# Kernel tuning notes

Hardware: AMD Instinct MI355X
Metric: run time of the kernel (lower is better)

## Reference

```python
import jax, jax.numpy as jnp
import numpy as np

# --- constants matching DILConfig ---
N_DIFF = 1000      # num_diffusion_steps
STEPS = 4          # inference_steps
S_MAX = 4          # max_scales
BUDGET = 0.2       # entropy_budget
G0 = 2.0           # guidance_strength
ENT_LO = 0.1       # stability_threshold_low
ENT_HI = 0.5       # stability_threshold_high
B, L, C, H = 16, 1024, 128, 512


def setup_inputs() -> dict:
    key = jax.random.key(0)
    ks = jax.random.split(key, 6)
    y_obs = jax.random.normal(ks[0], (B, L, C), dtype=jnp.float32)
    mask = (jax.random.uniform(ks[1], (B, L, C)) > 0.5).astype(jnp.float32)
    z_init = jax.random.normal(ks[2], (B, L, C), dtype=jnp.float32)
    W1 = jax.random.normal(ks[3], (C, H), dtype=jnp.float32) / np.sqrt(C)
    b1 = jnp.zeros((H,), dtype=jnp.float32)
    W2 = jax.random.normal(ks[4], (H, C), dtype=jnp.float32) / np.sqrt(H)
    b2 = jnp.zeros((C,), dtype=jnp.float32)
    tw = jax.random.normal(ks[5], (H,), dtype=jnp.float32)
    return {"y_obs": y_obs, "mask": mask, "z_init": z_init,
            "W1": W1, "b1": b1, "W2": W2, "b2": b2, "tw": tw}


def _dil_forward(y_obs, mask, z_init, W1, b1, W2, b2, tw):
    # diffusion schedule (linear betas)
    betas = jnp.linspace(1e-4, 0.02, N_DIFF, dtype=jnp.float32)
    ac = jnp.cumprod(1.0 - betas)
    alpha = jnp.sqrt(ac)                     # sqrt_alphas_cumprod
    sigma = jnp.sqrt(1.0 - ac)               # sqrt_one_minus_alphas_cumprod
    lam = jnp.log(alpha) - jnp.log(sigma)    # log-SNR/2

    step = N_DIFF // STEPS
    ks = [N_DIFF - 1 - i * step for i in range(STEPS)]

    def score(z, k):
        # epsilon predictor: channel MLP with scalar time feature
        t_feat = jnp.float32(k) / N_DIFF
        h = jax.nn.gelu(jnp.einsum('blc,ch->blh', z, W1) + b1 + t_feat * tw)
        return jnp.einsum('blh,hc->blc', h, W2) + b2

    z = z_init
    for k in ks:  # fixed small unrolled loop over inference steps
        kp = max(k - step, 0)
        eps = score(z, k)                                   # [B,L,C]
        h_lam = lam[kp] - lam[k]
        base_a = alpha[kp] / alpha[k]
        base_b = sigma[kp] * (jnp.exp(h_lam) - 1.0)

        # entropy map: batch-mean |eps| per pixel
        ent_pix = jnp.mean(jnp.abs(eps), axis=0)            # [L,C]

        # self-guidance on observed entries
        obs_err = (z - y_obs) * mask
        guidance = -obs_err / (jnp.var(obs_err) + 1e-8)     # [B,L,C]

        z_new = z
        # coarse -> fine so finer-scale selected nodes overwrite coarser ones
        for s in range(S_MAX - 1, -1, -1):
            w = 2 ** s
            pooled = ent_pix.reshape(L // w, w, C // w, w).mean(axis=(1, 3))
            Knodes = max(1, int(BUDGET * pooled.size))
            _, idx = jax.lax.top_k(pooled.ravel(), Knodes)
            selg = jnp.zeros((pooled.size,), jnp.float32).at[idx].set(1.0)
            selg = selg.reshape(pooled.shape)
            sel = jnp.repeat(jnp.repeat(selg, w, axis=0), w, axis=1)     # [L,C]
            ent_up = jnp.repeat(jnp.repeat(pooled, w, axis=0), w, axis=1)

            # adaptive solver order from entropy stability thresholds
            order = (1.0 + (ent_up > ENT_LO).astype(jnp.float32)
                         + (ent_up > ENT_HI).astype(jnp.float32))
            corr = (1.0 + (order - 1.0) * 0.5 * h_lam
                        + (order - 1.0) * (order - 2.0) / 6.0 * h_lam ** 2)
            gs = G0 * ent_up / (ent_up + 1.0)               # adaptive guidance

            cand = base_a * z - base_b * (corr * eps) + gs * guidance
            z_new = jnp.where(sel[None, :, :] > 0, cand, z_new)
        z = z_new
    return z


def reference(y_obs, mask, z_init, W1, b1, W2, b2, tw):
    return _dil_forward(y_obs, mask, z_init, W1, b1, W2, b2, tw)
```

## Files before the change

kernel.cpp:

```cpp
#include <hip/hip_runtime.h>
#include <math.h>
#include <stdint.h>

#define L_DIM 1024
#define C_DIM 128
#define H_DIM 512
#define B_DIM 16
#define LC (L_DIM * C_DIM)
#define BLC (B_DIM * LC)
#define M_DIM (B_DIM * L_DIM)

typedef __attribute__((ext_vector_type(8))) short short8;
typedef __attribute__((ext_vector_type(4))) float floatx4;

__device__ __forceinline__ unsigned ford(float x) {
    unsigned u = __float_as_uint(x);
    return (u & 0x80000000u) ? ~u : (u | 0x80000000u);
}

__device__ __forceinline__ void split3(float x, unsigned& uh, unsigned& um,
                                       unsigned& ul) {
    uh = __float_as_uint(x);
    const float r1 = x - __uint_as_float(uh & 0xffff0000u);
    um = __float_as_uint(r1);
    const float r2 = r1 - __uint_as_float(um & 0xffff0000u);
    ul = __float_as_uint(r2);
}

__device__ __forceinline__ float gelu_fast(float x) {
    const float g = 0.7978845608028654f * (x + 0.044715f * x * x * x);
    const float e = __expf(2.0f * g);
    const float t = 1.0f - 2.0f / (e + 1.0f);
    return 0.5f * x * (1.0f + t);
}

__global__ __launch_bounds__(256) void wsplit_kernel(
    const float* __restrict__ W1, const float* __restrict__ W2,
    unsigned short* __restrict__ W1h, unsigned short* __restrict__ W1m,
    unsigned short* __restrict__ W1l, unsigned short* __restrict__ W2h,
    unsigned short* __restrict__ W2m, unsigned short* __restrict__ W2l) {
    const int t = blockIdx.x * 256 + threadIdx.x;
    unsigned uh, um, ul;
    if (t < 65536) {
        const int j = t & 7, lane = (t >> 3) & 63, nt = (t >> 9) & 31,
                  kt = (t >> 14) & 3;
        const int k = kt * 32 + (lane >> 4) * 8 + j;
        const int n = nt * 16 + (lane & 15);
        split3(W1[k * 512 + n], uh, um, ul);
        W1h[t] = (unsigned short)(uh >> 16);
        W1m[t] = (unsigned short)(um >> 16);
        W1l[t] = (unsigned short)(ul >> 16);
    } else {
        const int t2 = t - 65536;
        const int j = t2 & 7, lane = (t2 >> 3) & 63, nt = (t2 >> 9) & 7,
                  kt = (t2 >> 12) & 15;
        const int k = kt * 32 + (lane >> 4) * 8 + j;
        const int n = nt * 16 + (lane & 15);
        split3(W2[k * 128 + n], uh, um, ul);
        W2h[t2] = (unsigned short)(uh >> 16);
        W2m[t2] = (unsigned short)(um >> 16);
        W2l[t2] = (unsigned short)(ul >> 16);
    }
}

#define MFMA6(AH, AM, AL, BH, BM, BL, ACC)                                    \
    ACC = __builtin_amdgcn_mfma_f32_16x16x32_bf16(AL, BH, ACC, 0, 0, 0);      \
    ACC = __builtin_amdgcn_mfma_f32_16x16x32_bf16(AM, BM, ACC, 0, 0, 0);      \
    ACC = __builtin_amdgcn_mfma_f32_16x16x32_bf16(AH, BL, ACC, 0, 0, 0);      \
    ACC = __builtin_amdgcn_mfma_f32_16x16x32_bf16(AM, BH, ACC, 0, 0, 0);      \
    ACC = __builtin_amdgcn_mfma_f32_16x16x32_bf16(AH, BM, ACC, 0, 0, 0);      \
    ACC = __builtin_amdgcn_mfma_f32_16x16x32_bf16(AH, BH, ACC, 0, 0, 0);

__device__ __forceinline__ void ldsA(const unsigned* hm,
                                     const unsigned short* lr, int row,
                                     int kbase, short8& Ah, short8& Am,
                                     short8& Al) {
    const unsigned* p = &hm[row * 132 + kbase];
    const uint4 a = *(const uint4*)p;
    const uint4 b = *(const uint4*)(p + 4);
    union { short8 v; unsigned u[4]; } ah, am;
    ah.u[0] = (a.x & 0xffffu) | (a.y << 16);
    ah.u[1] = (a.z & 0xffffu) | (a.w << 16);
    ah.u[2] = (b.x & 0xffffu) | (b.y << 16);
    ah.u[3] = (b.z & 0xffffu) | (b.w << 16);
    am.u[0] = (a.x >> 16) | (a.y & 0xffff0000u);
    am.u[1] = (a.z >> 16) | (a.w & 0xffff0000u);
    am.u[2] = (b.x >> 16) | (b.y & 0xffff0000u);
    am.u[3] = (b.z >> 16) | (b.w & 0xffff0000u);
    Ah = ah.v;
    Am = am.v;
    Al = *(const short8*)(&lr[row * 136 + kbase]);
}

__global__ __launch_bounds__(512, 2) void mlp_kernel(
    const float* __restrict__ z, const float* __restrict__ y,
    const float* __restrict__ mk,
    const unsigned short* __restrict__ W1h, const unsigned short* __restrict__ W1m,
    const unsigned short* __restrict__ W1l, const unsigned short* __restrict__ W2h,
    const unsigned short* __restrict__ W2m, const unsigned short* __restrict__ W2l,
    const float* __restrict__ b1, const float* __restrict__ tw,
    const float* __restrict__ b2, float t_feat,
    float* __restrict__ eps_out, float* __restrict__ ent,
    float* __restrict__ accum) {
    __shared__ unsigned z_hm[32 * 132];
    __shared__ unsigned short z_l[32 * 136];
    __shared__ unsigned h_hm[32 * 132];
    __shared__ unsigned short h_l[32 * 136];
    __shared__ float red1[8], red2[8];
    const int tid = threadIdx.x;
    const int w = tid >> 6, lane = tid & 63;
    const int quad = lane >> 4, m16 = lane & 15;
    const int l0 = blockIdx.x * 2;

#pragma unroll
    for (int e = 0; e < 2; ++e) {
        const int f = tid * 8 + e * 4;
        const int r = f >> 7, c = f & 127;
        const int b = r & 15, il = r >> 4;
        const float4 v = *(const float4*)(z + ((size_t)b * 1024 + l0 + il) * 128 + c);
        const float xs[4] = {v.x, v.y, v.z, v.w};
#pragma unroll
        for (int i = 0; i < 4; ++i) {
            unsigned uh, um, ul;
            split3(xs[i], uh, um, ul);
            z_hm[r * 132 + c + i] = (uh >> 16) | (um & 0xffff0000u);
            z_l[r * 136 + c + i] = (unsigned short)(ul >> 16);
        }
    }
    __syncthreads();

    floatx4 acc2[2];
    acc2[0] = (floatx4){0.f, 0.f, 0.f, 0.f};
    acc2[1] = (floatx4){0.f, 0.f, 0.f, 0.f};

    for (int hf = 0; hf < 2; ++hf) {
        floatx4 acc1[4];
#pragma unroll
        for (int i = 0; i < 4; ++i) acc1[i] = (floatx4){0.f, 0.f, 0.f, 0.f};

#pragma unroll
        for (int kt = 0; kt < 4; ++kt) {
            short8 Ah[2], Am[2], Al[2];
#pragma unroll
            for (int il = 0; il < 2; ++il)
                ldsA(z_hm, z_l, il * 16 + m16, kt * 32 + quad * 8,
                     Ah[il], Am[il], Al[il]);
#pragma unroll
            for (int s = 0; s < 2; ++s) {
                const int nt1 = (hf * 2 + s) * 8 + w;
                const size_t off = ((size_t)(kt * 32 + nt1) * 64 + lane) * 8;
                const short8 bh = *(const short8*)(W1h + off);
                const short8 bm = *(const short8*)(W1m + off);
                const short8 bl = *(const short8*)(W1l + off);
#pragma unroll
                for (int il = 0; il < 2; ++il) {
                    floatx4 a = acc1[s * 2 + il];
                    MFMA6(Ah[il], Am[il], Al[il], bh, bm, bl, a);
                    acc1[s * 2 + il] = a;
                }
            }
        }

#pragma unroll
        for (int s = 0; s < 2; ++s) {
            const int q = hf * 2 + s;
            __syncthreads();
            {
                const int coll = w * 16 + m16;
                const int colg = q * 128 + coll;
                const float bb = b1[colg] + t_feat * tw[colg];
#pragma unroll
                for (int il = 0; il < 2; ++il) {
#pragma unroll
                    for (int r = 0; r < 4; ++r) {
                        const float x = gelu_fast(acc1[s * 2 + il][r] + bb);
                        unsigned uh, um, ul;
                        split3(x, uh, um, ul);
                        const int row = il * 16 + quad * 4 + r;
                        h_hm[row * 132 + coll] = (uh >> 16) | (um & 0xffff0000u);
                        h_l[row * 136 + coll] = (unsigned short)(ul >> 16);
                    }
                }
            }
            __syncthreads();

#pragma unroll
            for (int ktl = 0; ktl < 4; ++ktl) {
                short8 Ah2[2], Am2[2], Al2[2];
#pragma unroll
                for (int il = 0; il < 2; ++il)
                    ldsA(h_hm, h_l, il * 16 + m16, ktl * 32 + quad * 8,
                         Ah2[il], Am2[il], Al2[il]);
                const int ktg = q * 4 + ktl;
                const size_t off = ((size_t)(ktg * 8 + w) * 64 + lane) * 8;
                const short8 bh = *(const short8*)(W2h + off);
                const short8 bm = *(const short8*)(W2m + off);
                const short8 bl = *(const short8*)(W2l + off);
#pragma unroll
                for (int il = 0; il < 2; ++il) {
                    floatx4 a = acc2[il];
                    MFMA6(Ah2[il], Am2[il], Al2[il], bh, bm, bl, a);
                    acc2[il] = a;
                }
            }
        }
    }

    {
        const int col = w * 16 + m16;
        const float bb2 = b2[col];
#pragma unroll
        for (int il = 0; il < 2; ++il) {
            float pa = 0.f;
#pragma unroll
            for (int r = 0; r < 4; ++r) {
                const float e = acc2[il][r] + bb2;
                const int b = quad * 4 + r;
                eps_out[((size_t)b * 1024 + l0 + il) * 128 + col] = e;
                pa += fabsf(e);
            }
            pa += __shfl_xor(pa, 16);
            pa += __shfl_xor(pa, 32);
            if (quad == 0) ent[(l0 + il) * 128 + col] = pa * (1.0f / 16.0f);
        }
    }

    float s1 = 0.f, s2 = 0.f;
#pragma unroll
    for (int e = 0; e < 2; ++e) {
        const int f = tid * 8 + e * 4;
        const int r = f >> 7, c = f & 127;
        const int b = r & 15, il = r >> 4;
        const size_t g = ((size_t)b * 1024 + l0 + il) * 128 + c;
        const float4 zv = *(const float4*)(z + g);
        const float4 yv = *(const float4*)(y + g);
        const float4 mv = *(const float4*)(mk + g);
        float oe;
        oe = (zv.x - yv.x) * mv.x; s1 += oe; s2 += oe * oe;
        oe = (zv.y - yv.y) * mv.y; s1 += oe; s2 += oe * oe;
        oe = (zv.z - yv.z) * mv.z; s1 += oe; s2 += oe * oe;
        oe = (zv.w - yv.w) * mv.w; s1 += oe; s2 += oe * oe;
    }
#pragma unroll
    for (int off = 32; off; off >>= 1) {
        s1 += __shfl_down(s1, off);
        s2 += __shfl_down(s2, off);
    }
    if (lane == 0) { red1[w] = s1; red2[w] = s2; }
    __syncthreads();
    if (tid == 0) {
        float a1 = 0.f, a2 = 0.f;
#pragma unroll
        for (int i = 0; i < 8; ++i) { a1 += red1[i]; a2 += red2[i]; }
        atomicAdd(&accum[0], a1);
        atomicAdd(&accum[1], a2);
    }
}

__global__ __launch_bounds__(256) void pool_kernel(
    const float* __restrict__ ent, float* __restrict__ p1,
    float* __restrict__ p2, float* __restrict__ p3) {
    const int idx = blockIdx.x * 256 + threadIdx.x;
    if (idx < 32768) {
        const int r = idx >> 6, c = idx & 63;
        float s = 0.f;
#pragma unroll
        for (int i = 0; i < 2; ++i)
#pragma unroll
            for (int j = 0; j < 2; ++j) s += ent[((r * 2 + i) << 7) + c * 2 + j];
        p1[idx] = s * 0.25f;
    } else if (idx < 40960) {
        const int t = idx - 32768;
        const int r = t >> 5, c = t & 31;
        float s = 0.f;
#pragma unroll
        for (int i = 0; i < 4; ++i)
#pragma unroll
            for (int j = 0; j < 4; ++j) s += ent[((r * 4 + i) << 7) + c * 4 + j];
        p2[t] = s * 0.0625f;
    } else {
        const int t = idx - 40960;
        const int r = t >> 4, c = t & 15;
        float s = 0.f;
#pragma unroll
        for (int i = 0; i < 8; ++i)
#pragma unroll
            for (int j = 0; j < 8; ++j) s += ent[((r * 8 + i) << 7) + c * 8 + j];
        p3[t] = s * (1.0f / 64.0f);
    }
}

__global__ __launch_bounds__(256) void hist_kernel(
    const float* __restrict__ e0, const float* __restrict__ e1,
    const float* __restrict__ e2, const float* __restrict__ e3,
    unsigned* __restrict__ ghist, unsigned* __restrict__ gprefix,
    unsigned* __restrict__ gkrem, unsigned* __restrict__ dctr, int shift) {
    const int bid = blockIdx.x;
    const float* data;
    int scale, base;
    if (bid < 64) { scale = 0; data = e0; base = bid * 2048; }
    else if (bid < 80) { scale = 1; data = e1; base = (bid - 64) * 2048; }
    else if (bid < 84) { scale = 2; data = e2; base = (bid - 80) * 2048; }
    else { scale = 3; data = e3; base = 0; }

    __shared__ unsigned hist[4][256];
    __shared__ unsigned sh[256];
    __shared__ bool sh_last;
    const int t = threadIdx.x;
    const int w = t >> 6;
#pragma unroll
    for (int i = t; i < 1024; i += 256) ((unsigned*)hist)[i] = 0u;
    __syncthreads();

    const unsigned prefix = gprefix[scale];
    const unsigned hmask = (shift == 24) ? 0u : (0xFFFFFFFFu << (shift + 8));

#pragma unroll
    for (int i = t; i < 2048; i += 256) {
        const unsigned u = ford(data[base + i]);
        if ((u & hmask) == (prefix & hmask))
            atomicAdd(&hist[w][(u >> shift) & 255u], 1u);
    }
    __syncthreads();
    const unsigned c = hist[0][t] + hist[1][t] + hist[2][t] + hist[3][t];
    if (c) atomicAdd(&ghist[scale * 256 + t], c);
    __syncthreads();

    if (t == 0) {
        __threadfence();
        sh_last = (atomicAdd(dctr, 1u) == 84u);
    }
    __syncthreads();
    if (!sh_last) return;

    __threadfence();
    const unsigned Kc[4] = {26214u, 6553u, 1638u, 409u};
#pragma unroll
    for (int s = 0; s < 4; ++s) {
        sh[t] = atomicAdd(&ghist[s * 256 + t], 0u);
        __syncthreads();
#pragma unroll
        for (int off = 1; off < 256; off <<= 1) {
            const unsigned v = (t + off < 256) ? sh[t + off] : 0u;
            __syncthreads();
            sh[t] += v;
            __syncthreads();
        }
        const unsigned suf = sh[t];
        const unsigned sufn = (t < 255) ? sh[t + 1] : 0u;
        const unsigned krem = (shift == 24) ? Kc[s] : gkrem[s];
        const unsigned pref = (shift == 24) ? 0u : gprefix[s];
        if (suf >= krem && sufn < krem) {
            gprefix[s] = pref | ((unsigned)t << shift);
            gkrem[s] = krem - sufn;
        }
        ghist[s * 256 + t] = 0u;
        __syncthreads();
    }
}

__global__ __launch_bounds__(256) void update_kernel(
    float* __restrict__ z, const float* __restrict__ y,
    const float* __restrict__ mk, const float* __restrict__ eps,
    const float* __restrict__ ent, const float* __restrict__ p1,
    const float* __restrict__ p2, const float* __restrict__ p3,
    const unsigned* __restrict__ thr, const float* __restrict__ accum,
    float base_a, float base_b, float h_lam) {
    const int idx = blockIdx.x * 256 + threadIdx.x;
    const int p = idx & (LC - 1);
    const int l = p >> 7;
    const int c = p & 127;

    const float mean = accum[0] * (1.0f / (float)BLC);
    const float var = accum[1] * (1.0f / (float)BLC) - mean * mean;

    const float zi = z[idx];
    const float oe = (zi - y[idx]) * mk[idx];
    const float guid = -oe / (var + 1e-8f);
    const float ei = eps[idx];

    float ent_v = 0.f;
    bool sel = false;
    {
        const float v0 = ent[p];
        if (ford(v0) >= thr[0]) { ent_v = v0; sel = true; }
        else {
            const float v1 = p1[((l >> 1) << 6) + (c >> 1)];
            if (ford(v1) >= thr[1]) { ent_v = v1; sel = true; }
            else {
                const float v2 = p2[((l >> 2) << 5) + (c >> 2)];
                if (ford(v2) >= thr[2]) { ent_v = v2; sel = true; }
                else {
                    const float v3 = p3[((l >> 3) << 4) + (c >> 3)];
                    if (ford(v3) >= thr[3]) { ent_v = v3; sel = true; }
                }
            }
        }
    }
    if (sel) {
        float corr;
        if (ent_v > 0.5f)
            corr = 1.0f + h_lam + h_lam * h_lam * (1.0f / 3.0f);
        else if (ent_v > 0.1f)
            corr = 1.0f + 0.5f * h_lam;
        else
            corr = 1.0f;
        const float gs = 2.0f * ent_v / (ent_v + 1.0f);
        z[idx] = base_a * zi - base_b * (corr * ei) + gs * guid;
    }
}

extern "C" void kernel_launch(void* const* d_in, const int* in_sizes, int n_in,
                              void* d_out, int out_size, void* d_ws,
                              size_t ws_size, hipStream_t stream) {
    const float* y_obs = (const float*)d_in[0];
    const float* mask = (const float*)d_in[1];
    const float* z_init = (const float*)d_in[2];
    const float* W1 = (const float*)d_in[3];
    const float* b1 = (const float*)d_in[4];
    const float* W2 = (const float*)d_in[5];
    const float* b2 = (const float*)d_in[6];
    const float* tw = (const float*)d_in[7];
    float* z = (float*)d_out;
    float* ws = (float*)d_ws;

    float* eps = ws;
    float* ent = ws + 2097152;
    float* p1 = ws + 2228224;
    float* p2 = ws + 2260992;
    float* p3 = ws + 2269184;
    unsigned* ghist = (unsigned*)(ws + 2271232);
    unsigned* done = (unsigned*)(ws + 2272256);
    float* accum = ws + 2272272;
    unsigned* gprefix = (unsigned*)(ws + 2272280);
    unsigned* gkrem = (unsigned*)(ws + 2272284);
    unsigned short* W1h = (unsigned short*)(ws + 2272288);
    unsigned short* W1m = (unsigned short*)(ws + 2305056);
    unsigned short* W1l = (unsigned short*)(ws + 2337824);
    unsigned short* W2h = (unsigned short*)(ws + 2370592);
    unsigned short* W2m = (unsigned short*)(ws + 2403360);
    unsigned short* W2l = (unsigned short*)(ws + 2436128);

    float alpha_[1000], sigma_[1000], lam_[1000];
    {
        float ac = 1.0f;
        for (int i = 0; i < 1000; ++i) {
            const float beta = 1e-4f + (0.02f - 1e-4f) * ((float)i / 999.0f);
            ac = ac * (1.0f - beta);
            alpha_[i] = sqrtf(ac);
            sigma_[i] = sqrtf(1.0f - ac);
            lam_[i] = logf(alpha_[i]) - logf(sigma_[i]);
        }
    }

    hipMemcpyAsync(z, z_init, sizeof(float) * BLC, hipMemcpyDeviceToDevice,
                   stream);
    hipMemsetAsync(ghist, 0, (1024 + 16 + 8) * sizeof(unsigned), stream);
    wsplit_kernel<<<512, 256, 0, stream>>>(W1, W2, W1h, W1m, W1l, W2h, W2m,
                                           W2l);

    for (int si = 0; si < 4; ++si) {
        const int k = 999 - si * 250;
        const int kp = (k - 250 > 0) ? (k - 250) : 0;
        const float t_feat = (float)k / 1000.0f;
        const float h_lam = lam_[kp] - lam_[k];
        const float base_a = alpha_[kp] / alpha_[k];
        const float base_b = sigma_[kp] * (expf(h_lam) - 1.0f);

        mlp_kernel<<<512, 512, 0, stream>>>(
            z, y_obs, mask, W1h, W1m, W1l, W2h, W2m, W2l, b1, tw, b2, t_feat,
            eps, ent, accum + 2 * si);
        pool_kernel<<<168, 256, 0, stream>>>(ent, p1, p2, p3);
        int pass = 0;
        for (int shift = 24; shift >= 0; shift -= 8, ++pass) {
            hist_kernel<<<85, 256, 0, stream>>>(ent, p1, p2, p3, ghist,
                                                gprefix, gkrem,
                                                done + si * 4 + pass, shift);
        }
        update_kernel<<<8192, 256, 0, stream>>>(z, y_obs, mask, eps, ent, p1,
                                                p2, p3, gprefix, accum + 2 * si,
                                                base_a, base_b, h_lam);
    }
}
```

Baseline: 457.4 us.

## Fuse update into next MLP step and merge pool/histogram passes with grid barrier

The per-step z update moves into the next step's MLP kernel prologue, which is templated on whether to apply it. This saves a full pass over z, y, mask and eps for three of the four steps. Pooling and the four radix-select histogram passes merge into one persistent 85-block kernel synchronised by a software grid barrier, replacing five launches per step. The LDS A-operand layout is also changed to store hi/mid/lo bf16 planes pre-swizzled for direct short8 loads, removing the unpacking shuffles. The grid barrier relies on all 85 blocks being co-resident, and it adds atomic traffic for the reads and writes of the pooled values.

```diff
diff --git a/kernel.cpp b/kernel.cpp
--- a/kernel.cpp
+++ b/kernel.cpp
@@ -8,13 +8,15 @@
 #define B_DIM 16
 #define LC (L_DIM * C_DIM)
 #define BLC (B_DIM * LC)
-#define M_DIM (B_DIM * L_DIM)
 
 typedef __attribute__((ext_vector_type(8))) short short8;
 typedef __attribute__((ext_vector_type(4))) float floatx4;
 
 __device__ __forceinline__ unsigned ford(float x) {
     unsigned u = __float_as_uint(x);
+    return (u & 0x80000000u) ? ~u : (u | 0x80000000u);
+}
+__device__ __forceinline__ unsigned fordbits(unsigned u) {
     return (u & 0x80000000u) ? ~u : (u | 0x80000000u);
 }
 
@@ -71,63 +73,125 @@
     ACC = __builtin_amdgcn_mfma_f32_16x16x32_bf16(AH, BM, ACC, 0, 0, 0);      \
     ACC = __builtin_amdgcn_mfma_f32_16x16x32_bf16(AH, BH, ACC, 0, 0, 0);
 
-__device__ __forceinline__ void ldsA(const unsigned* hm,
-                                     const unsigned short* lr, int row,
-                                     int kbase, short8& Ah, short8& Am,
-                                     short8& Al) {
-    const unsigned* p = &hm[row * 132 + kbase];
-    const uint4 a = *(const uint4*)p;
-    const uint4 b = *(const uint4*)(p + 4);
-    union { short8 v; unsigned u[4]; } ah, am;
-    ah.u[0] = (a.x & 0xffffu) | (a.y << 16);
-    ah.u[1] = (a.z & 0xffffu) | (a.w << 16);
-    ah.u[2] = (b.x & 0xffffu) | (b.y << 16);
-    ah.u[3] = (b.z & 0xffffu) | (b.w << 16);
-    am.u[0] = (a.x >> 16) | (a.y & 0xffff0000u);
-    am.u[1] = (a.z >> 16) | (a.w & 0xffff0000u);
-    am.u[2] = (b.x >> 16) | (b.y & 0xffff0000u);
-    am.u[3] = (b.z >> 16) | (b.w & 0xffff0000u);
-    Ah = ah.v;
-    Am = am.v;
-    Al = *(const short8*)(&lr[row * 136 + kbase]);
-}
-
+__device__ __forceinline__ float upd_elem(
+    float zi, float yi, float mi, float ei, int l, int c,
+    const float* __restrict__ ent, const float* __restrict__ p1,
+    const float* __restrict__ p2, const float* __restrict__ p3,
+    unsigned t0, unsigned t1, unsigned t2, unsigned t3, float var,
+    float base_a, float base_b, float h_lam) {
+    float ent_v = 0.f;
+    bool sel = false;
+    const float v0 = ent[l * 128 + c];
+    if (ford(v0) >= t0) { ent_v = v0; sel = true; }
+    else {
+        const float v1 = p1[((l >> 1) << 6) + (c >> 1)];
+        if (ford(v1) >= t1) { ent_v = v1; sel = true; }
+        else {
+            const float v2 = p2[((l >> 2) << 5) + (c >> 2)];
+            if (ford(v2) >= t2) { ent_v = v2; sel = true; }
+            else {
+                const float v3 = p3[((l >> 3) << 4) + (c >> 3)];
+                if (ford(v3) >= t3) { ent_v = v3; sel = true; }
+            }
+        }
+    }
+    if (!sel) return zi;
+    float corr;
+    if (ent_v > 0.5f) corr = 1.0f + h_lam + h_lam * h_lam * (1.0f / 3.0f);
+    else if (ent_v > 0.1f) corr = 1.0f + 0.5f * h_lam;
+    else corr = 1.0f;
+    const float gs = 2.0f * ent_v / (ent_v + 1.0f);
+    const float oe = (zi - yi) * mi;
+    const float guid = -oe / (var + 1e-8f);
+    return base_a * zi - base_b * (corr * ei) + gs * guid;
+}
+
+template <int UPD>
 __global__ __launch_bounds__(512, 2) void mlp_kernel(
-    const float* __restrict__ z, const float* __restrict__ y,
+    float* __restrict__ z, const float* __restrict__ y,
     const float* __restrict__ mk,
     const unsigned short* __restrict__ W1h, const unsigned short* __restrict__ W1m,
     const unsigned short* __restrict__ W1l, const unsigned short* __restrict__ W2h,
     const unsigned short* __restrict__ W2m, const unsigned short* __restrict__ W2l,
     const float* __restrict__ b1, const float* __restrict__ tw,
     const float* __restrict__ b2, float t_feat,
-    float* __restrict__ eps_out, float* __restrict__ ent,
-    float* __restrict__ accum) {
-    __shared__ unsigned z_hm[32 * 132];
-    __shared__ unsigned short z_l[32 * 136];
-    __shared__ unsigned h_hm[32 * 132];
-    __shared__ unsigned short h_l[32 * 136];
+    float* __restrict__ eps_buf, float* __restrict__ ent,
+    const float* __restrict__ p1, const float* __restrict__ p2,
+    const float* __restrict__ p3, const unsigned* __restrict__ gpref,
+    const float* __restrict__ accumPrev, float* __restrict__ accum,
+    float base_a, float base_b, float h_lam) {
+    __shared__ unsigned short zA[3][4096];
+    __shared__ unsigned short hA[3][4096];
     __shared__ float red1[8], red2[8];
     const int tid = threadIdx.x;
     const int w = tid >> 6, lane = tid & 63;
     const int quad = lane >> 4, m16 = lane & 15;
     const int l0 = blockIdx.x * 2;
 
+    float var = 0.f;
+    unsigned t0 = 0, t1 = 0, t2 = 0, t3 = 0;
+    if (UPD) {
+        const float mean = accumPrev[0] * (1.0f / (float)BLC);
+        var = accumPrev[1] * (1.0f / (float)BLC) - mean * mean;
+        t0 = gpref[0]; t1 = gpref[1]; t2 = gpref[2]; t3 = gpref[3];
+    }
+
+    float s1 = 0.f, s2 = 0.f;
 #pragma unroll
     for (int e = 0; e < 2; ++e) {
         const int f = tid * 8 + e * 4;
-        const int r = f >> 7, c = f & 127;
-        const int b = r & 15, il = r >> 4;
-        const float4 v = *(const float4*)(z + ((size_t)b * 1024 + l0 + il) * 128 + c);
-        const float xs[4] = {v.x, v.y, v.z, v.w};
-#pragma unroll
-        for (int i = 0; i < 4; ++i) {
-            unsigned uh, um, ul;
-            split3(xs[i], uh, um, ul);
-            z_hm[r * 132 + c + i] = (uh >> 16) | (um & 0xffff0000u);
-            z_l[r * 136 + c + i] = (unsigned short)(ul >> 16);
-        }
-    }
+        const int r_ = f >> 7, cb = f & 127;
+        const int b = r_ & 15, il = r_ >> 4, l = l0 + il;
+        const size_t g = ((size_t)b * 1024 + l) * 128 + cb;
+        float4 zv = *(const float4*)(z + g);
+        const float4 yv = *(const float4*)(y + g);
+        const float4 mv = *(const float4*)(mk + g);
+        if (UPD) {
+            const float4 ev = *(const float4*)(eps_buf + g);
+            zv.x = upd_elem(zv.x, yv.x, mv.x, ev.x, l, cb + 0, ent, p1, p2, p3,
+                            t0, t1, t2, t3, var, base_a, base_b, h_lam);
+            zv.y = upd_elem(zv.y, yv.y, mv.y, ev.y, l, cb + 1, ent, p1, p2, p3,
+                            t0, t1, t2, t3, var, base_a, base_b, h_lam);
+            zv.z = upd_elem(zv.z, yv.z, mv.z, ev.z, l, cb + 2, ent, p1, p2, p3,
+                            t0, t1, t2, t3, var, base_a, base_b, h_lam);
+            zv.w = upd_elem(zv.w, yv.w, mv.w, ev.w, l, cb + 3, ent, p1, p2, p3,
+                            t0, t1, t2, t3, var, base_a, base_b, h_lam);
+            *(float4*)(z + g) = zv;
+        }
+        float oe;
+        oe = (zv.x - yv.x) * mv.x; s1 += oe; s2 += oe * oe;
+        oe = (zv.y - yv.y) * mv.y; s1 += oe; s2 += oe * oe;
+        oe = (zv.z - yv.z) * mv.z; s1 += oe; s2 += oe * oe;
+        oe = (zv.w - yv.w) * mv.w; s1 += oe; s2 += oe * oe;
+
+        const int kt = cb >> 5;
+        const int fi = ((kt * 2 + il) * 64 + ((cb >> 3) & 3) * 16 + b) * 8 +
+                       (cb & 7);
+        const float xs[4] = {zv.x, zv.y, zv.z, zv.w};
+        ushort4 vh, vm, vl;
+        unsigned uh, um, ul;
+        split3(xs[0], uh, um, ul); vh.x = uh >> 16; vm.x = um >> 16; vl.x = ul >> 16;
+        split3(xs[1], uh, um, ul); vh.y = uh >> 16; vm.y = um >> 16; vl.y = ul >> 16;
+        split3(xs[2], uh, um, ul); vh.z = uh >> 16; vm.z = um >> 16; vl.z = ul >> 16;
+        split3(xs[3], uh, um, ul); vh.w = uh >> 16; vm.w = um >> 16; vl.w = ul >> 16;
+        *(ushort4*)(&zA[0][fi]) = vh;
+        *(ushort4*)(&zA[1][fi]) = vm;
+        *(ushort4*)(&zA[2][fi]) = vl;
+    }
+#pragma unroll
+    for (int off = 32; off; off >>= 1) {
+        s1 += __shfl_down(s1, off);
+        s2 += __shfl_down(s2, off);
+    }
+    if (lane == 0) { red1[w] = s1; red2[w] = s2; }
     __syncthreads();
+    if (tid == 0) {
+        float a1 = 0.f, a2 = 0.f;
+#pragma unroll
+        for (int i = 0; i < 8; ++i) { a1 += red1[i]; a2 += red2[i]; }
+        atomicAdd(&accum[0], a1);
+        atomicAdd(&accum[1], a2);
+    }
 
     floatx4 acc2[2];
     acc2[0] = (floatx4){0.f, 0.f, 0.f, 0.f};
@@ -142,9 +206,12 @@
         for (int kt = 0; kt < 4; ++kt) {
             short8 Ah[2], Am[2], Al[2];
 #pragma unroll
-            for (int il = 0; il < 2; ++il)
-                ldsA(z_hm, z_l, il * 16 + m16, kt * 32 + quad * 8,
-                     Ah[il], Am[il], Al[il]);
+            for (int il = 0; il < 2; ++il) {
+                const int fb = ((kt * 2 + il) * 64 + lane) * 8;
+                Ah[il] = *(const short8*)(&zA[0][fb]);
+                Am[il] = *(const short8*)(&zA[1][fb]);
+                Al[il] = *(const short8*)(&zA[2][fb]);
+            }
 #pragma unroll
             for (int s = 0; s < 2; ++s) {
                 const int nt1 = (hf * 2 + s) * 8 + w;
@@ -166,9 +233,11 @@
             const int q = hf * 2 + s;
             __syncthreads();
             {
-                const int coll = w * 16 + m16;
-                const int colg = q * 128 + coll;
+                const int colg = q * 128 + w * 16 + m16;
                 const float bb = b1[colg] + t_feat * tw[colg];
+                const int ib = ((w >> 1) * 2) * 64 * 8;
+                const int l2b = (((w & 1) << 1) | (m16 >> 3)) * 16;
+                const int jj = m16 & 7;
 #pragma unroll
                 for (int il = 0; il < 2; ++il) {
 #pragma unroll
@@ -176,9 +245,11 @@
                         const float x = gelu_fast(acc1[s * 2 + il][r] + bb);
                         unsigned uh, um, ul;
                         split3(x, uh, um, ul);
-                        const int row = il * 16 + quad * 4 + r;
-                        h_hm[row * 132 + coll] = (uh >> 16) | (um & 0xffff0000u);
-                        h_l[row * 136 + coll] = (unsigned short)(ul >> 16);
+                        const int idx =
+                            ib + il * 512 + (l2b + quad * 4 + r) * 8 + jj;
+                        hA[0][idx] = (unsigned short)(uh >> 16);
+                        hA[1][idx] = (unsigned short)(um >> 16);
+                        hA[2][idx] = (unsigned short)(ul >> 16);
                     }
                 }
             }
@@ -188,9 +259,12 @@
             for (int ktl = 0; ktl < 4; ++ktl) {
                 short8 Ah2[2], Am2[2], Al2[2];
 #pragma unroll
-                for (int il = 0; il < 2; ++il)
-                    ldsA(h_hm, h_l, il * 16 + m16, ktl * 32 + quad * 8,
-                         Ah2[il], Am2[il], Al2[il]);
+                for (int il = 0; il < 2; ++il) {
+                    const int fb = ((ktl * 2 + il) * 64 + lane) * 8;
+                    Ah2[il] = *(const short8*)(&hA[0][fb]);
+                    Am2[il] = *(const short8*)(&hA[1][fb]);
+                    Al2[il] = *(const short8*)(&hA[2][fb]);
+                }
                 const int ktg = q * 4 + ktl;
                 const size_t off = ((size_t)(ktg * 8 + w) * 64 + lane) * 8;
                 const short8 bh = *(const short8*)(W2h + off);
@@ -216,7 +290,7 @@
             for (int r = 0; r < 4; ++r) {
                 const float e = acc2[il][r] + bb2;
                 const int b = quad * 4 + r;
-                eps_out[((size_t)b * 1024 + l0 + il) * 128 + col] = e;
+                eps_buf[((size_t)b * 1024 + l0 + il) * 128 + col] = e;
                 pa += fabsf(e);
             }
             pa += __shfl_xor(pa, 16);
@@ -224,120 +298,97 @@
             if (quad == 0) ent[(l0 + il) * 128 + col] = pa * (1.0f / 16.0f);
         }
     }
-
-    float s1 = 0.f, s2 = 0.f;
-#pragma unroll
-    for (int e = 0; e < 2; ++e) {
-        const int f = tid * 8 + e * 4;
-        const int r = f >> 7, c = f & 127;
-        const int b = r & 15, il = r >> 4;
-        const size_t g = ((size_t)b * 1024 + l0 + il) * 128 + c;
-        const float4 zv = *(const float4*)(z + g);
-        const float4 yv = *(const float4*)(y + g);
-        const float4 mv = *(const float4*)(mk + g);
-        float oe;
-        oe = (zv.x - yv.x) * mv.x; s1 += oe; s2 += oe * oe;
-        oe = (zv.y - yv.y) * mv.y; s1 += oe; s2 += oe * oe;
-        oe = (zv.z - yv.z) * mv.z; s1 += oe; s2 += oe * oe;
-        oe = (zv.w - yv.w) * mv.w; s1 += oe; s2 += oe * oe;
-    }
-#pragma unroll
-    for (int off = 32; off; off >>= 1) {
-        s1 += __shfl_down(s1, off);
-        s2 += __shfl_down(s2, off);
-    }
-    if (lane == 0) { red1[w] = s1; red2[w] = s2; }
+}
+
+__device__ __forceinline__ void grid_barrier(unsigned* ctr, unsigned* rel,
+                                             unsigned target) {
     __syncthreads();
-    if (tid == 0) {
-        float a1 = 0.f, a2 = 0.f;
-#pragma unroll
-        for (int i = 0; i < 8; ++i) { a1 += red1[i]; a2 += red2[i]; }
-        atomicAdd(&accum[0], a1);
-        atomicAdd(&accum[1], a2);
-    }
-}
-
-__global__ __launch_bounds__(256) void pool_kernel(
+    if (threadIdx.x == 0) {
+        __threadfence();
+        if (atomicAdd(ctr, 1u) + 1u == target) {
+            atomicExch(rel, target);
+        } else {
+            while (atomicAdd(rel, 0u) < target) __builtin_amdgcn_s_sleep(8);
+        }
+    }
+    __syncthreads();
+}
+
+__global__ __launch_bounds__(256, 1) void select_kernel(
     const float* __restrict__ ent, float* __restrict__ p1,
-    float* __restrict__ p2, float* __restrict__ p3) {
-    const int idx = blockIdx.x * 256 + threadIdx.x;
-    if (idx < 32768) {
-        const int r = idx >> 6, c = idx & 63;
+    float* __restrict__ p2, float* __restrict__ p3,
+    unsigned* __restrict__ ghist, unsigned* __restrict__ ctr,
+    unsigned* __restrict__ rel, unsigned* __restrict__ gprefix, int si) {
+    const int bid = blockIdx.x, t = threadIdx.x;
+    const int gid = bid * 256 + t;
+    const unsigned target0 = (unsigned)(si * 5) * 85u;
+
+    for (int i = gid; i < 32768; i += 21760) {
+        const int r = i >> 6, c = i & 63;
         float s = 0.f;
 #pragma unroll
-        for (int i = 0; i < 2; ++i)
-#pragma unroll
-            for (int j = 0; j < 2; ++j) s += ent[((r * 2 + i) << 7) + c * 2 + j];
-        p1[idx] = s * 0.25f;
-    } else if (idx < 40960) {
-        const int t = idx - 32768;
-        const int r = t >> 5, c = t & 31;
+        for (int ii = 0; ii < 2; ++ii)
+#pragma unroll
+            for (int jj = 0; jj < 2; ++jj)
+                s += ent[((r * 2 + ii) << 7) + c * 2 + jj];
+        atomicExch((unsigned*)&p1[i], __float_as_uint(s * 0.25f));
+    }
+    for (int i = gid; i < 8192; i += 21760) {
+        const int r = i >> 5, c = i & 31;
         float s = 0.f;
 #pragma unroll
-        for (int i = 0; i < 4; ++i)
-#pragma unroll
-            for (int j = 0; j < 4; ++j) s += ent[((r * 4 + i) << 7) + c * 4 + j];
-        p2[t] = s * 0.0625f;
-    } else {
-        const int t = idx - 40960;
-        const int r = t >> 4, c = t & 15;
+        for (int ii = 0; ii < 4; ++ii)
+#pragma unroll
+            for (int jj = 0; jj < 4; ++jj)
+                s += ent[((r * 4 + ii) << 7) + c * 4 + jj];
+        atomicExch((unsigned*)&p2[i], __float_as_uint(s * 0.0625f));
+    }
+    for (int i = gid; i < 2048; i += 21760) {
+        const int r = i >> 4, c = i & 15;
         float s = 0.f;
 #pragma unroll
-        for (int i = 0; i < 8; ++i)
-#pragma unroll
-            for (int j = 0; j < 8; ++j) s += ent[((r * 8 + i) << 7) + c * 8 + j];
-        p3[t] = s * (1.0f / 64.0f);
-    }
-}
-
-__global__ __launch_bounds__(256) void hist_kernel(
-    const float* __restrict__ e0, const float* __restrict__ e1,
-    const float* __restrict__ e2, const float* __restrict__ e3,
-    unsigned* __restrict__ ghist, unsigned* __restrict__ gprefix,
-    unsigned* __restrict__ gkrem, unsigned* __restrict__ dctr, int shift) {
-    const int bid = blockIdx.x;
+        for (int ii = 0; ii < 8; ++ii)
+#pragma unroll
+            for (int jj = 0; jj < 8; ++jj)
+                s += ent[((r * 8 + ii) << 7) + c * 8 + jj];
+        atomicExch((unsigned*)&p3[i], __float_as_uint(s * (1.0f / 64.0f)));
+    }
+    grid_barrier(ctr, rel, target0 + 85u);
+
     const float* data;
     int scale, base;
-    if (bid < 64) { scale = 0; data = e0; base = bid * 2048; }
-    else if (bid < 80) { scale = 1; data = e1; base = (bid - 64) * 2048; }
-    else if (bid < 84) { scale = 2; data = e2; base = (bid - 80) * 2048; }
-    else { scale = 3; data = e3; base = 0; }
+    unsigned K;
+    if (bid < 64) { scale = 0; data = ent; base = bid * 2048; K = 26214u; }
+    else if (bid < 80) { scale = 1; data = p1; base = (bid - 64) * 2048; K = 6553u; }
+    else if (bid < 84) { scale = 2; data = p2; base = (bid - 80) * 2048; K = 1638u; }
+    else { scale = 3; data = p3; base = 0; K = 409u; }
 
     __shared__ unsigned hist[4][256];
     __shared__ unsigned sh[256];
-    __shared__ bool sh_last;
-    const int t = threadIdx.x;
-    const int w = t >> 6;
-#pragma unroll
-    for (int i = t; i < 1024; i += 256) ((unsigned*)hist)[i] = 0u;
-    __syncthreads();
-
-    const unsigned prefix = gprefix[scale];
-    const unsigned hmask = (shift == 24) ? 0u : (0xFFFFFFFFu << (shift + 8));
-
-#pragma unroll
-    for (int i = t; i < 2048; i += 256) {
-        const unsigned u = ford(data[base + i]);
-        if ((u & hmask) == (prefix & hmask))
-            atomicAdd(&hist[w][(u >> shift) & 255u], 1u);
-    }
-    __syncthreads();
-    const unsigned c = hist[0][t] + hist[1][t] + hist[2][t] + hist[3][t];
-    if (c) atomicAdd(&ghist[scale * 256 + t], c);
-    __syncthreads();
-
-    if (t == 0) {
-        __threadfence();
-        sh_last = (atomicAdd(dctr, 1u) == 84u);
-    }
-    __syncthreads();
-    if (!sh_last) return;
-
-    __threadfence();
-    const unsigned Kc[4] = {26214u, 6553u, 1638u, 409u};
-#pragma unroll
-    for (int s = 0; s < 4; ++s) {
-        sh[t] = atomicAdd(&ghist[s * 256 + t], 0u);
+    __shared__ unsigned sh_dig, sh_krem;
+    const int wv = t >> 6;
+    unsigned prefix = 0u, krem = K;
+
+    for (int p = 0; p < 4; ++p) {
+        const int shift = 24 - 8 * p;
+        const unsigned hmask = p ? (0xFFFFFFFFu << (shift + 8)) : 0u;
+#pragma unroll
+        for (int i = t; i < 1024; i += 256) ((unsigned*)hist)[i] = 0u;
+        __syncthreads();
+#pragma unroll
+        for (int i = t; i < 2048; i += 256) {
+            const unsigned raw =
+                atomicAdd((unsigned*)&data[base + i], 0u);
+            const unsigned u = fordbits(raw);
+            if ((u & hmask) == (prefix & hmask))
+                atomicAdd(&hist[wv][(u >> shift) & 255u], 1u);
+        }
+        __syncthreads();
+        const unsigned c = hist[0][t] + hist[1][t] + hist[2][t] + hist[3][t];
+        unsigned* gh = &ghist[((si * 4 + p) * 4 + scale) * 256];
+        if (c) atomicAdd(&gh[t], c);
+        grid_barrier(ctr, rel, target0 + 85u * (unsigned)(p + 2));
+        sh[t] = atomicAdd(&gh[t], 0u);
         __syncthreads();
 #pragma unroll
         for (int off = 1; off < 256; off <<= 1) {
@@ -348,15 +399,16 @@
         }
         const unsigned suf = sh[t];
         const unsigned sufn = (t < 255) ? sh[t + 1] : 0u;
-        const unsigned krem = (shift == 24) ? Kc[s] : gkrem[s];
-        const unsigned pref = (shift == 24) ? 0u : gprefix[s];
         if (suf >= krem && sufn < krem) {
-            gprefix[s] = pref | ((unsigned)t << shift);
-            gkrem[s] = krem - sufn;
-        }
-        ghist[s * 256 + t] = 0u;
+            sh_dig = (unsigned)t;
+            sh_krem = krem - sufn;
+        }
         __syncthreads();
-    }
+        prefix |= (sh_dig << shift);
+        krem = sh_krem;
+        __syncthreads();
+    }
+    if (t == 0 && base == 0) gprefix[scale] = prefix;
 }
 
 __global__ __launch_bounds__(256) void update_kernel(
@@ -370,44 +422,12 @@
     const int p = idx & (LC - 1);
     const int l = p >> 7;
     const int c = p & 127;
-
     const float mean = accum[0] * (1.0f / (float)BLC);
     const float var = accum[1] * (1.0f / (float)BLC) - mean * mean;
-
     const float zi = z[idx];
-    const float oe = (zi - y[idx]) * mk[idx];
-    const float guid = -oe / (var + 1e-8f);
-    const float ei = eps[idx];
-
-    float ent_v = 0.f;
-    bool sel = false;
-    {
-        const float v0 = ent[p];
-        if (ford(v0) >= thr[0]) { ent_v = v0; sel = true; }
-        else {
-            const float v1 = p1[((l >> 1) << 6) + (c >> 1)];
-            if (ford(v1) >= thr[1]) { ent_v = v1; sel = true; }
-            else {
-                const float v2 = p2[((l >> 2) << 5) + (c >> 2)];
-                if (ford(v2) >= thr[2]) { ent_v = v2; sel = true; }
-                else {
-                    const float v3 = p3[((l >> 3) << 4) + (c >> 3)];
-                    if (ford(v3) >= thr[3]) { ent_v = v3; sel = true; }
-                }
-            }
-        }
-    }
-    if (sel) {
-        float corr;
-        if (ent_v > 0.5f)
-            corr = 1.0f + h_lam + h_lam * h_lam * (1.0f / 3.0f);
-        else if (ent_v > 0.1f)
-            corr = 1.0f + 0.5f * h_lam;
-        else
-            corr = 1.0f;
-        const float gs = 2.0f * ent_v / (ent_v + 1.0f);
-        z[idx] = base_a * zi - base_b * (corr * ei) + gs * guid;
-    }
+    z[idx] = upd_elem(zi, y[idx], mk[idx], eps[idx], l, c, ent, p1, p2, p3,
+                      thr[0], thr[1], thr[2], thr[3], var, base_a, base_b,
+                      h_lam);
 }
 
 extern "C" void kernel_launch(void* const* d_in, const int* in_sizes, int n_in,
@@ -430,16 +450,16 @@
     float* p2 = ws + 2260992;
     float* p3 = ws + 2269184;
     unsigned* ghist = (unsigned*)(ws + 2271232);
-    unsigned* done = (unsigned*)(ws + 2272256);
-    float* accum = ws + 2272272;
-    unsigned* gprefix = (unsigned*)(ws + 2272280);
-    unsigned* gkrem = (unsigned*)(ws + 2272284);
-    unsigned short* W1h = (unsigned short*)(ws + 2272288);
-    unsigned short* W1m = (unsigned short*)(ws + 2305056);
-    unsigned short* W1l = (unsigned short*)(ws + 2337824);
-    unsigned short* W2h = (unsigned short*)(ws + 2370592);
-    unsigned short* W2m = (unsigned short*)(ws + 2403360);
-    unsigned short* W2l = (unsigned short*)(ws + 2436128);
+    unsigned* ctr = (unsigned*)(ws + 2287616);
+    unsigned* rel = (unsigned*)(ws + 2287617);
+    float* accum = ws + 2287618;
+    unsigned* gprefix = (unsigned*)(ws + 2287626);
+    unsigned short* W1h = (unsigned short*)(ws + 2287632);
+    unsigned short* W1m = (unsigned short*)(ws + 2320400);
+    unsigned short* W1l = (unsigned short*)(ws + 2353168);
+    unsigned short* W2h = (unsigned short*)(ws + 2385936);
+    unsigned short* W2m = (unsigned short*)(ws + 2418704);
+    unsigned short* W2l = (unsigned short*)(ws + 2451472);
 
     float alpha_[1000], sigma_[1000], lam_[1000];
     {
@@ -452,33 +472,38 @@
             lam_[i] = logf(alpha_[i]) - logf(sigma_[i]);
         }
     }
-
-    hipMemcpyAsync(z, z_init, sizeof(float) * BLC, hipMemcpyDeviceToDevice,
-                   stream);
-    hipMemsetAsync(ghist, 0, (1024 + 16 + 8) * sizeof(unsigned), stream);
-    wsplit_kernel<<<512, 256, 0, stream>>>(W1, W2, W1h, W1m, W1l, W2h, W2m,
-                                           W2l);
-
+    float tf[4], hl[4], ba[4], bb[4];
     for (int si = 0; si < 4; ++si) {
         const int k = 999 - si * 250;
         const int kp = (k - 250 > 0) ? (k - 250) : 0;
-        const float t_feat = (float)k / 1000.0f;
-        const float h_lam = lam_[kp] - lam_[k];
-        const float base_a = alpha_[kp] / alpha_[k];
-        const float base_b = sigma_[kp] * (expf(h_lam) - 1.0f);
-
-        mlp_kernel<<<512, 512, 0, stream>>>(
-            z, y_obs, mask, W1h, W1m, W1l, W2h, W2m, W2l, b1, tw, b2, t_feat,
-            eps, ent, accum + 2 * si);
-        pool_kernel<<<168, 256, 0, stream>>>(ent, p1, p2, p3);
-        int pass = 0;
-        for (int shift = 24; shift >= 0; shift -= 8, ++pass) {
-            hist_kernel<<<85, 256, 0, stream>>>(ent, p1, p2, p3, ghist,
-                                                gprefix, gkrem,
-                                                done + si * 4 + pass, shift);
-        }
-        update_kernel<<<8192, 256, 0, stream>>>(z, y_obs, mask, eps, ent, p1,
-                                                p2, p3, gprefix, accum + 2 * si,
-                                                base_a, base_b, h_lam);
-    }
-}
+        tf[si] = (float)k / 1000.0f;
+        hl[si] = lam_[kp] - lam_[k];
+        ba[si] = alpha_[kp] / alpha_[k];
+        bb[si] = sigma_[kp] * (expf(hl[si]) - 1.0f);
+    }
+
+    hipMemcpyAsync(z, z_init, sizeof(float) * BLC, hipMemcpyDeviceToDevice,
+                   stream);
+    hipMemsetAsync(ghist, 0, (16384 + 2 + 8 + 4) * sizeof(unsigned), stream);
+    wsplit_kernel<<<512, 256, 0, stream>>>(W1, W2, W1h, W1m, W1l, W2h, W2m,
+                                           W2l);
+
+    for (int si = 0; si < 4; ++si) {
+        if (si == 0) {
+            mlp_kernel<0><<<512, 512, 0, stream>>>(
+                z, y_obs, mask, W1h, W1m, W1l, W2h, W2m, W2l, b1, tw, b2,
+                tf[0], eps, ent, p1, p2, p3, gprefix, accum, accum, 0.f, 0.f,
+                0.f);
+        } else {
+            mlp_kernel<1><<<512, 512, 0, stream>>>(
+                z, y_obs, mask, W1h, W1m, W1l, W2h, W2m, W2l, b1, tw, b2,
+                tf[si], eps, ent, p1, p2, p3, gprefix, accum + 2 * (si - 1),
+                accum + 2 * si, ba[si - 1], bb[si - 1], hl[si - 1]);
+        }
+        select_kernel<<<85, 256, 0, stream>>>(ent, p1, p2, p3, ghist, ctr, rel,
+                                              gprefix, si);
+    }
+    update_kernel<<<8192, 256, 0, stream>>>(z, y_obs, mask, eps, ent, p1, p2,
+                                            p3, gprefix, accum + 6, ba[3],
+                                            bb[3], hl[3]);
+}
```

After: 505.6 us. 10.5% more time.
